# Performance work log

Measured on AMD Instinct MI355X. Metric: run time of the kernel, lower is better.

## Reference

```python
import jax, jax.numpy as jnp
import numpy as np

ALPHA = 0.2  # LeakyReLU negative slope
MASK_FILL = -9e15


def setup_inputs() -> dict:
    key = jax.random.key(0)
    k1, k2, k3, k4 = jax.random.split(key, 4)
    N, F_IN, F_OUT = 8192, 128, 64
    x = jax.random.normal(k1, (N, F_IN), dtype=jnp.float32)
    adj = jax.random.randint(k2, (N, N), 0, 2, dtype=jnp.int32)
    # xavier_uniform with gain=1.414 (approx sqrt(2))
    gain = 1.414
    lim_w = gain * np.sqrt(6.0 / (F_IN + F_OUT))
    W = jax.random.uniform(k3, (F_IN, F_OUT), minval=-lim_w, maxval=lim_w, dtype=jnp.float32)
    lim_a = gain * np.sqrt(6.0 / (2 * F_OUT + 1))
    a = jax.random.uniform(k4, (2 * F_OUT, 1), minval=-lim_a, maxval=lim_a, dtype=jnp.float32)
    return {"x": x, "adj": adj, "W": W, "a": a}


def reference(x, adj, W, a):
    # h: [N, F_out]
    h = x @ W
    f_out = h.shape[1]
    # Decompose a^T [h_i || h_j] = h_i . a1 + h_j . a2 (exactly the same math,
    # avoids materializing the N*N*2F concat tensor).
    a1 = a[:f_out, 0]  # [F_out]
    a2 = a[f_out:, 0]  # [F_out]
    e = (h @ a1)[:, None] + (h @ a2)[None, :]  # [N, N]
    e = jax.nn.leaky_relu(e, negative_slope=ALPHA)
    e = jnp.where(adj > 0, e, MASK_FILL)
    attention = jax.nn.softmax(e, axis=1)  # row-wise softmax
    h_prime = attention @ h  # [N, F_out]
    return jax.nn.elu(h_prime)  # concat=True branch
```

## Files before the change

### kernel.cpp

```cpp
#include <hip/hip_runtime.h>
#include <math.h>

#define NN 8192
#define FIN 128
#define FOUT 64
#define LRELU 0.2f
#define JSPLIT 32
#define JCH (NN / JSPLIT)
#define HTSTR 264
#define L2E 1.44269504f

typedef _Float16 f16x8 __attribute__((ext_vector_type(8)));
typedef float f32x4 __attribute__((ext_vector_type(4)));

#define WS_HT 0
#define WS_S1 262144
#define WS_S2 270336
#define WS_S2MAX 278528
#define WS_PACC 278544
#define WS_LP (WS_PACC + JSPLIT * NN * FOUT)

__global__ __launch_bounds__(256) void k_hs(const float* __restrict__ x,
                                            const float* __restrict__ W,
                                            const float* __restrict__ a,
                                            float* ws) {
  __shared__ float Wl[FIN * FOUT];
  __shared__ float xl[16 * FIN];
  __shared__ float hl[16 * FOUT];
  const int t = threadIdx.x;
  const int i0 = blockIdx.x * 16;

#pragma unroll
  for (int c = 0; c < 8; ++c) {
    const int flat = c * 1024 + t * 4;
    *(float4*)&Wl[flat] = *(const float4*)&W[flat];
  }
#pragma unroll
  for (int c = 0; c < 2; ++c) {
    const int flat = c * 1024 + t * 4;
    *(float4*)&xl[flat] = *(const float4*)&x[(size_t)i0 * FIN + flat];
  }
  __syncthreads();

  const int r = t >> 4;
  const int fg = t & 15;
  float4 acc = make_float4(0.f, 0.f, 0.f, 0.f);
#pragma unroll 4
  for (int k = 0; k < FIN; ++k) {
    const float xv = xl[r * FIN + k];
    const float4 wv = *(const float4*)&Wl[k * FOUT + fg * 4];
    acc.x = fmaf(xv, wv.x, acc.x);
    acc.y = fmaf(xv, wv.y, acc.y);
    acc.z = fmaf(xv, wv.z, acc.z);
    acc.w = fmaf(xv, wv.w, acc.w);
  }

  float v1 = acc.x * a[fg * 4] + acc.y * a[fg * 4 + 1] +
             acc.z * a[fg * 4 + 2] + acc.w * a[fg * 4 + 3];
  float v2 = acc.x * a[FOUT + fg * 4] + acc.y * a[FOUT + fg * 4 + 1] +
             acc.z * a[FOUT + fg * 4 + 2] + acc.w * a[FOUT + fg * 4 + 3];
  v1 += __shfl_xor(v1, 1); v2 += __shfl_xor(v2, 1);
  v1 += __shfl_xor(v1, 2); v2 += __shfl_xor(v2, 2);
  v1 += __shfl_xor(v1, 4); v2 += __shfl_xor(v2, 4);
  v1 += __shfl_xor(v1, 8); v2 += __shfl_xor(v2, 8);
  if (fg == 0) {
    ws[WS_S1 + i0 + r] = v1;
    ws[WS_S2 + i0 + r] = v2;
  }

  *(float4*)&hl[r * FOUT + fg * 4] = acc;
  __syncthreads();
  _Float16* ht = (_Float16*)(ws + WS_HT);
  if (t < 128) {
    const int f = t >> 1;
    const int off = (t & 1) * 8;
    f16x8 tmp;
#pragma unroll
    for (int u = 0; u < 8; ++u) tmp[u] = (_Float16)hl[(off + u) * FOUT + f];
    *(f16x8*)&ht[(size_t)f * NN + i0 + off] = tmp;
  }
}

__global__ __launch_bounds__(256) void k_s2max(float* ws) {
  __shared__ float red[256];
  const int t = threadIdx.x;
  float v = -1e30f;
#pragma unroll
  for (int i = 0; i < NN / 256; ++i) v = fmaxf(v, ws[WS_S2 + i * 256 + t]);
  red[t] = v;
  __syncthreads();
  for (int s = 128; s >= 1; s >>= 1) {
    if (t < s) red[t] = fmaxf(red[t], red[t + s]);
    __syncthreads();
  }
  if (t == 0) ws[WS_S2MAX] = red[0];
}

__global__ __launch_bounds__(256, 4) void k_main(const int* __restrict__ adj,
                                                 float* ws) {
  __shared__ __align__(16) _Float16 htl[FOUT * HTSTR];
  __shared__ float s2l[JCH];

  const int t = threadIdx.x;
  const int ib = blockIdx.x >> 5;
  const int js = blockIdx.x & 31;
  const int i0 = ib * 64;
  const int jc0 = js * JCH;

  const _Float16* ht = (const _Float16*)(ws + WS_HT);

#pragma unroll
  for (int c = 0; c < 8; ++c) {
    const int chunk = c * 256 + t;
    const int f = chunk >> 5;
    const int off = (chunk & 31) * 8;
    *(f16x8*)&htl[f * HTSTR + off] = *(const f16x8*)&ht[(size_t)f * NN + jc0 + off];
  }
  s2l[t] = ws[WS_S2 + jc0 + t];

  const int w = t >> 6;
  const int l = t & 63;
  const int m16 = l & 15;
  const int q8 = (l >> 4) * 8;
  const int row = i0 + w * 16 + m16;

  const float s2max = ws[WS_S2MAX];
  const float s1v = ws[WS_S1 + row];
  const float tmp0 = s1v + s2max;
  const float mv = fmaxf(tmp0, LRELU * tmp0);
  const float mneg = -mv * L2E;

  f32x4 acc[4];
#pragma unroll
  for (int nf = 0; nf < 4; ++nf) acc[nf] = (f32x4){0.f, 0.f, 0.f, 0.f};
  float lacc = 0.f;

  const int* arow = adj + (size_t)row * NN + jc0 + q8;

  __syncthreads();

#pragma unroll 4
  for (int it = 0; it < JCH / 32; ++it) {
    const int4 a0 = *(const int4*)(arow + it * 32);
    const int4 a1 = *(const int4*)(arow + it * 32 + 4);
    const float4 s20 = *(const float4*)&s2l[it * 32 + q8];
    const float4 s21 = *(const float4*)&s2l[it * 32 + q8 + 4];

    float e, p[8];
    e = s1v + s20.x; e = fmaxf(e, LRELU * e); p[0] = a0.x ? exp2f(fmaf(e, L2E, mneg)) : 0.f;
    e = s1v + s20.y; e = fmaxf(e, LRELU * e); p[1] = a0.y ? exp2f(fmaf(e, L2E, mneg)) : 0.f;
    e = s1v + s20.z; e = fmaxf(e, LRELU * e); p[2] = a0.z ? exp2f(fmaf(e, L2E, mneg)) : 0.f;
    e = s1v + s20.w; e = fmaxf(e, LRELU * e); p[3] = a0.w ? exp2f(fmaf(e, L2E, mneg)) : 0.f;
    e = s1v + s21.x; e = fmaxf(e, LRELU * e); p[4] = a1.x ? exp2f(fmaf(e, L2E, mneg)) : 0.f;
    e = s1v + s21.y; e = fmaxf(e, LRELU * e); p[5] = a1.y ? exp2f(fmaf(e, L2E, mneg)) : 0.f;
    e = s1v + s21.z; e = fmaxf(e, LRELU * e); p[6] = a1.z ? exp2f(fmaf(e, L2E, mneg)) : 0.f;
    e = s1v + s21.w; e = fmaxf(e, LRELU * e); p[7] = a1.w ? exp2f(fmaf(e, L2E, mneg)) : 0.f;

    f16x8 af;
#pragma unroll
    for (int u = 0; u < 8; ++u) af[u] = (_Float16)p[u];
#pragma unroll
    for (int u = 0; u < 8; ++u) lacc += (float)af[u];

    const int kb = it * 32 + q8;
#pragma unroll
    for (int nf = 0; nf < 4; ++nf) {
      const f16x8 b = *(const f16x8*)&htl[(nf * 16 + m16) * HTSTR + kb];
      acc[nf] = __builtin_amdgcn_mfma_f32_16x16x32_f16(af, b, acc[nf], 0, 0, 0);
    }
  }

  lacc += __shfl_xor(lacc, 16);
  lacc += __shfl_xor(lacc, 32);
  if (l < 16) ws[WS_LP + js * NN + row] = lacc;

  float* pacc = ws + WS_PACC + (size_t)js * (NN * FOUT);
  const int orow = i0 + w * 16 + (l >> 4) * 4;
  const int ocol = m16;
#pragma unroll
  for (int nf = 0; nf < 4; ++nf)
#pragma unroll
    for (int r = 0; r < 4; ++r)
      pacc[(size_t)(orow + r) * FOUT + nf * 16 + ocol] = acc[nf][r];
}

__global__ __launch_bounds__(256) void k_combine(const float* __restrict__ ws,
                                                 float* __restrict__ out) {
  const int idx = blockIdx.x * 256 + threadIdx.x;
  const int i = idx >> 6;
  float s = 0.f, l = 0.f;
#pragma unroll
  for (int js = 0; js < JSPLIT; ++js) {
    s += ws[WS_PACC + (size_t)js * (NN * FOUT) + idx];
    l += ws[WS_LP + js * NN + i];
  }
  const float v = s / l;
  out[idx] = v > 0.f ? v : expm1f(v);
}

extern "C" void kernel_launch(void* const* d_in, const int* in_sizes, int n_in,
                              void* d_out, int out_size, void* d_ws,
                              size_t ws_size, hipStream_t stream) {
  const float* x = (const float*)d_in[0];
  const int* adj = (const int*)d_in[1];
  const float* W = (const float*)d_in[2];
  const float* a = (const float*)d_in[3];
  float* ws = (float*)d_ws;
  float* out = (float*)d_out;

  hipLaunchKernelGGL(k_hs, dim3(NN / 16), dim3(256), 0, stream, x, W, a, ws);
  hipLaunchKernelGGL(k_s2max, dim3(1), dim3(256), 0, stream, ws);
  hipLaunchKernelGGL(k_main, dim3((NN / 64) * JSPLIT), dim3(256), 0, stream,
                     adj, ws);
  hipLaunchKernelGGL(k_combine, dim3(NN * FOUT / 256), dim3(256), 0, stream,
                     ws, out);
}
```

Before: 399.8 us.

## Stage adjacency-derived probabilities in LDS with coalesced row-wise adj loads

```diff
diff --git a/kernel.cpp b/kernel.cpp
--- a/kernel.cpp
+++ b/kernel.cpp
@@ -8,9 +8,11 @@
 #define JSPLIT 32
 #define JCH (NN / JSPLIT)
 #define HTSTR 264
+#define PSTRH 264
 #define L2E 1.44269504f
 
 typedef _Float16 f16x8 __attribute__((ext_vector_type(8)));
+typedef _Float16 f16x4 __attribute__((ext_vector_type(4)));
 typedef float f32x4 __attribute__((ext_vector_type(4)));
 
 #define WS_HT 0
@@ -96,10 +98,10 @@
   if (t == 0) ws[WS_S2MAX] = red[0];
 }
 
-__global__ __launch_bounds__(256, 4) void k_main(const int* __restrict__ adj,
+__global__ __launch_bounds__(256, 2) void k_main(const int* __restrict__ adj,
                                                  float* ws) {
+  __shared__ __align__(16) _Float16 pal[64 * PSTRH];
   __shared__ __align__(16) _Float16 htl[FOUT * HTSTR];
-  __shared__ float s2l[JCH];
 
   const int t = threadIdx.x;
   const int ib = blockIdx.x >> 5;
@@ -116,53 +118,49 @@
     const int off = (chunk & 31) * 8;
     *(f16x8*)&htl[f * HTSTR + off] = *(const f16x8*)&ht[(size_t)f * NN + jc0 + off];
   }
-  s2l[t] = ws[WS_S2 + jc0 + t];
 
   const int w = t >> 6;
   const int l = t & 63;
+  const float s2max = ws[WS_S2MAX];
+  const float4 s2v = *(const float4*)&ws[WS_S2 + jc0 + l * 4];
+
+#pragma unroll
+  for (int s = 0; s < 16; ++s) {
+    const int rl = w * 16 + s;
+    const float s1v = ws[WS_S1 + i0 + rl];
+    const float tm = s1v + s2max;
+    const float mv = fmaxf(tm, LRELU * tm);
+    const float mneg = -mv * L2E;
+    const int4 av = *(const int4*)&adj[(size_t)(i0 + rl) * NN + jc0 + l * 4];
+    float e;
+    e = s1v + s2v.x; e = fmaxf(e, LRELU * e);
+    const _Float16 p0 = av.x ? (_Float16)exp2f(fmaf(e, L2E, mneg)) : (_Float16)0.f;
+    e = s1v + s2v.y; e = fmaxf(e, LRELU * e);
+    const _Float16 p1 = av.y ? (_Float16)exp2f(fmaf(e, L2E, mneg)) : (_Float16)0.f;
+    e = s1v + s2v.z; e = fmaxf(e, LRELU * e);
+    const _Float16 p2 = av.z ? (_Float16)exp2f(fmaf(e, L2E, mneg)) : (_Float16)0.f;
+    e = s1v + s2v.w; e = fmaxf(e, LRELU * e);
+    const _Float16 p3 = av.w ? (_Float16)exp2f(fmaf(e, L2E, mneg)) : (_Float16)0.f;
+    f16x4 pv = {p0, p1, p2, p3};
+    *(f16x4*)&pal[rl * PSTRH + l * 4] = pv;
+  }
+
+  __syncthreads();
+
   const int m16 = l & 15;
   const int q8 = (l >> 4) * 8;
-  const int row = i0 + w * 16 + m16;
-
-  const float s2max = ws[WS_S2MAX];
-  const float s1v = ws[WS_S1 + row];
-  const float tmp0 = s1v + s2max;
-  const float mv = fmaxf(tmp0, LRELU * tmp0);
-  const float mneg = -mv * L2E;
 
   f32x4 acc[4];
 #pragma unroll
   for (int nf = 0; nf < 4; ++nf) acc[nf] = (f32x4){0.f, 0.f, 0.f, 0.f};
   float lacc = 0.f;
 
-  const int* arow = adj + (size_t)row * NN + jc0 + q8;
-
-  __syncthreads();
-
-#pragma unroll 4
+#pragma unroll
   for (int it = 0; it < JCH / 32; ++it) {
-    const int4 a0 = *(const int4*)(arow + it * 32);
-    const int4 a1 = *(const int4*)(arow + it * 32 + 4);
-    const float4 s20 = *(const float4*)&s2l[it * 32 + q8];
-    const float4 s21 = *(const float4*)&s2l[it * 32 + q8 + 4];
-
-    float e, p[8];
-    e = s1v + s20.x; e = fmaxf(e, LRELU * e); p[0] = a0.x ? exp2f(fmaf(e, L2E, mneg)) : 0.f;
-    e = s1v + s20.y; e = fmaxf(e, LRELU * e); p[1] = a0.y ? exp2f(fmaf(e, L2E, mneg)) : 0.f;
-    e = s1v + s20.z; e = fmaxf(e, LRELU * e); p[2] = a0.z ? exp2f(fmaf(e, L2E, mneg)) : 0.f;
-    e = s1v + s20.w; e = fmaxf(e, LRELU * e); p[3] = a0.w ? exp2f(fmaf(e, L2E, mneg)) : 0.f;
-    e = s1v + s21.x; e = fmaxf(e, LRELU * e); p[4] = a1.x ? exp2f(fmaf(e, L2E, mneg)) : 0.f;
-    e = s1v + s21.y; e = fmaxf(e, LRELU * e); p[5] = a1.y ? exp2f(fmaf(e, L2E, mneg)) : 0.f;
-    e = s1v + s21.z; e = fmaxf(e, LRELU * e); p[6] = a1.z ? exp2f(fmaf(e, L2E, mneg)) : 0.f;
-    e = s1v + s21.w; e = fmaxf(e, LRELU * e); p[7] = a1.w ? exp2f(fmaf(e, L2E, mneg)) : 0.f;
-
-    f16x8 af;
-#pragma unroll
-    for (int u = 0; u < 8; ++u) af[u] = (_Float16)p[u];
+    const int kb = it * 32 + q8;
+    const f16x8 af = *(const f16x8*)&pal[(w * 16 + m16) * PSTRH + kb];
 #pragma unroll
     for (int u = 0; u < 8; ++u) lacc += (float)af[u];
-
-    const int kb = it * 32 + q8;
 #pragma unroll
     for (int nf = 0; nf < 4; ++nf) {
       const f16x8 b = *(const f16x8*)&htl[(nf * 16 + m16) * HTSTR + kb];
@@ -172,16 +170,15 @@
 
   lacc += __shfl_xor(lacc, 16);
   lacc += __shfl_xor(lacc, 32);
-  if (l < 16) ws[WS_LP + js * NN + row] = lacc;
+  if (l < 16) ws[WS_LP + js * NN + i0 + w * 16 + m16] = lacc;
 
   float* pacc = ws + WS_PACC + (size_t)js * (NN * FOUT);
   const int orow = i0 + w * 16 + (l >> 4) * 4;
-  const int ocol = m16;
 #pragma unroll
   for (int nf = 0; nf < 4; ++nf)
 #pragma unroll
     for (int r = 0; r < 4; ++r)
-      pacc[(size_t)(orow + r) * FOUT + nf * 16 + ocol] = acc[nf][r];
+      pacc[(size_t)(orow + r) * FOUT + nf * 16 + m16] = acc[nf][r];
 }
 
 __global__ __launch_bounds__(256) void k_combine(const float* __restrict__ ws,
```

Result: no change. 406.8 us (+1.8%).
